# Kernel optimization log

Measured on AMD Instinct MI355X. Metric: run time of the kernel, lower is better.

Reference implementation:

```python
import jax, jax.numpy as jnp
import numpy as np


def setup_inputs() -> dict:
    key = jax.random.key(0)
    k1, k2, k3, k4 = jax.random.split(key, 4)
    B, N, M, D = 8, 2048, 2048, 256
    x = jax.random.normal(k1, (B, N, D), dtype=jnp.float32)
    Fi = jax.random.normal(k2, (B, M, D), dtype=jnp.float32)
    # nn.Linear(dim, dim) params (W applied as x @ W.T + b); scale like torch default
    bound = 1.0 / np.sqrt(D)
    W = jax.random.uniform(k3, (D, D), dtype=jnp.float32, minval=-bound, maxval=bound)
    b = jax.random.uniform(k4, (D,), dtype=jnp.float32, minval=-bound, maxval=bound)
    return {"x": x, "Fi": Fi, "W": W, "b": b}


def reference(x, Fi, W, b):
    # x: [B, N, D], Fi: [B, M, D]
    q = jnp.einsum("bnd,ed->bne", x, W) + b          # linear projection
    scores = jnp.einsum("bnd,bmd->bnm", q, Fi)        # QK^T (no scaling in original)
    attn = jax.nn.softmax(scores, axis=-1)            # softmax over keys
    out = jnp.einsum("bnm,bmd->bnd", attn, Fi)        # attention @ V (V = Fi)
    return out
```

## Files before the change

kernel.cpp:

```cpp
#include <hip/hip_runtime.h>
#include <hip/hip_bf16.h>

typedef _Float16 half8 __attribute__((ext_vector_type(8)));
typedef float floatx4 __attribute__((ext_vector_type(4)));

#define MFMA16H(a, b, c) __builtin_amdgcn_mfma_f32_16x16x32_f16((a), (b), (c), 0, 0, 0)

static constexpr int Bb = 8, Nn = 2048, Mm = 2048, Dd = 256;

__device__ inline void async16(const void* g, void* l)
{
    __builtin_amdgcn_global_load_lds((const __attribute__((address_space(1))) unsigned int*)g,
                                     (__attribute__((address_space(3))) unsigned int*)l,
                                     16, 0, 0);
}

__device__ inline half8 cvt8h(const float* __restrict__ p)
{
    float4 f0 = *reinterpret_cast<const float4*>(p);
    float4 f1 = *reinterpret_cast<const float4*>(p + 4);
    half8 r;
    r[0] = (_Float16)f0.x; r[1] = (_Float16)f0.y; r[2] = (_Float16)f0.z; r[3] = (_Float16)f0.w;
    r[4] = (_Float16)f1.x; r[5] = (_Float16)f1.y; r[6] = (_Float16)f1.z; r[7] = (_Float16)f1.w;
    return r;
}

__device__ inline void cvt8h_split(const float* __restrict__ p, half8& h, half8& l)
{
    float4 f0 = *reinterpret_cast<const float4*>(p);
    float4 f1 = *reinterpret_cast<const float4*>(p + 4);
    float f[8] = {f0.x, f0.y, f0.z, f0.w, f1.x, f1.y, f1.z, f1.w};
#pragma unroll
    for (int i = 0; i < 8; ++i) {
        _Float16 hh = (_Float16)f[i];
        h[i] = hh;
        l[i] = (_Float16)(f[i] - (float)hh);
    }
}

__global__ __launch_bounds__(256, 4)
void prep_kernel(const float* __restrict__ Fi, const float* __restrict__ W,
                 _Float16* __restrict__ FiH, _Float16* __restrict__ FiT,
                 _Float16* __restrict__ Wh, _Float16* __restrict__ Wl)
{
    const int bid = blockIdx.x;
    const int t = threadIdx.x;

    if (bid >= 1024) {
        const size_t base = (size_t)(bid - 1024) * 2048 + t * 8;
        half8 h, l;
        cvt8h_split(W + base, h, l);
        *(half8*)(Wh + base) = h;
        *(half8*)(Wl + base) = l;
        return;
    }

    __shared__ __align__(16) unsigned short tile[64][64];
    const int b  = bid >> 7;
    const int mt = (bid >> 2) & 31;
    const int dt = bid & 3;
    {
        const int i = t >> 2, jc = (t & 3) * 16;
        const int pc = ((jc >> 4) ^ (i >> 4)) * 16;
        const float* src = Fi + ((size_t)b * Mm + mt * 64 + i) * Dd + dt * 64 + jc;
        union { half8 v; uint4 u; } p0, p1;
        p0.v = cvt8h(src);
        p1.v = cvt8h(src + 8);
        *(uint4*)&tile[i][pc]     = p0.u;
        *(uint4*)&tile[i][pc + 8] = p1.u;
        unsigned short* dh = reinterpret_cast<unsigned short*>(FiH)
            + ((size_t)b * Mm + mt * 64 + i) * Dd + dt * 64 + jc;
        *(uint4*)dh       = p0.u;
        *(uint4*)(dh + 8) = p1.u;
    }
    __syncthreads();
    {
        const int d = t >> 2, mc = (t & 3) * 16;
        unsigned short* dst = reinterpret_cast<unsigned short*>(FiT)
            + ((size_t)b * Dd + dt * 64 + d) * Mm + mt * 64 + mc;
        union { uint4 v[2]; unsigned short s[16]; } u;
#pragma unroll
        for (int s = 0; s < 16; ++s) {
            const int row = mc + s;
            u.s[s] = tile[row][((d >> 4) ^ (row >> 4)) * 16 + (d & 15)];
        }
        *(uint4*)dst       = u.v[0];
        *(uint4*)(dst + 8) = u.v[1];
    }
}

__global__ __launch_bounds__(256, 2)
void qproj_kernel(const float* __restrict__ x, const _Float16* __restrict__ Wh,
                  const _Float16* __restrict__ Wl, const float* __restrict__ bias,
                  _Float16* __restrict__ q)
{
    __shared__ __align__(16) _Float16 sWhA[256 * 32];
    __shared__ __align__(16) _Float16 sWlA[256 * 32];
    __shared__ __align__(16) _Float16 sWhB[256 * 32];
    __shared__ __align__(16) _Float16 sWlB[256 * 32];

    const int tid = threadIdx.x;
    const int lane = tid & 63, w = tid >> 6;
    const int lo = lane & 15, hi = lane >> 4;
    const long r0 = (long)blockIdx.x * 32;

    floatx4 acc[2][4];
#pragma unroll
    for (int rt = 0; rt < 2; ++rt)
#pragma unroll
        for (int j = 0; j < 4; ++j) acc[rt][j] = (floatx4)0.0f;

    const int se = lane >> 2, sc = lane & 3;

    auto stage = [&](int k0, _Float16* dWh, _Float16* dWl) {
#pragma unroll
        for (int j = 0; j < 4; ++j) {
            const int e0 = (w * 4 + j) * 16;
            const int e = e0 + se;
            const int gc = sc ^ (e & 3);
            async16(Wh + (size_t)e * Dd + k0 + gc * 8, dWh + e0 * 32);
            async16(Wl + (size_t)e * Dd + k0 + gc * 8, dWl + e0 * 32);
        }
    };

    auto compute = [&](int k0, const _Float16* SWh, const _Float16* SWl) {
        half8 ah[2], al[2];
#pragma unroll
        for (int rt = 0; rt < 2; ++rt)
            cvt8h_split(x + (size_t)(r0 + rt * 16 + lo) * Dd + k0 + hi * 8, ah[rt], al[rt]);
#pragma unroll
        for (int jj = 0; jj < 4; ++jj) {
            const int e = (w * 4 + jj) * 16 + lo;
            half8 bh = *reinterpret_cast<const half8*>(&SWh[(e & 255) * 32 + ((hi ^ (e & 3)) * 8)]);
            half8 bl = *reinterpret_cast<const half8*>(&SWl[(e & 255) * 32 + ((hi ^ (e & 3)) * 8)]);
#pragma unroll
            for (int rt = 0; rt < 2; ++rt) {
                acc[rt][jj] = MFMA16H(ah[rt], bh, acc[rt][jj]);
                acc[rt][jj] = MFMA16H(ah[rt], bl, acc[rt][jj]);
                acc[rt][jj] = MFMA16H(al[rt], bh, acc[rt][jj]);
            }
        }
    };

    stage(0, sWhA, sWlA);
    for (int k0 = 0; k0 < 256; k0 += 64) {
        __syncthreads();
        stage(k0 + 32, sWhB, sWlB);
        compute(k0, sWhA, sWlA);
        __syncthreads();
        if (k0 + 64 < 256) stage(k0 + 64, sWhA, sWlA);
        compute(k0 + 32, sWhB, sWlB);
    }
#pragma unroll
    for (int jj = 0; jj < 4; ++jj) {
        const int e = (w * 4 + jj) * 16 + lo;
        const float bv = bias[e];
#pragma unroll
        for (int rt = 0; rt < 2; ++rt)
#pragma unroll
            for (int r = 0; r < 4; ++r)
                q[(size_t)(r0 + rt * 16 + hi * 4 + r) * Dd + e] = (_Float16)(acc[rt][jj][r] + bv);
    }
}

__global__ __launch_bounds__(256, 2)
void flash_kernel(const _Float16* __restrict__ q, const _Float16* __restrict__ FiH,
                  const _Float16* __restrict__ FiT, _Float16* __restrict__ o_part,
                  float* __restrict__ m_part, float* __restrict__ l_part)
{
    __shared__ __align__(16) _Float16 sFiA[32 * 256];
    __shared__ __align__(16) _Float16 sFiB[32 * 256];
    __shared__ __align__(16) _Float16 sFiTA[256 * 32];
    __shared__ __align__(16) _Float16 sFiTB[256 * 32];
    __shared__ __align__(16) _Float16 sP[4][32 * 36];

    const int bid = blockIdx.x;
    const int b  = bid & 7;
    const int u  = bid >> 3;
    const int nt = u & 15;
    const int kh = u >> 4;
    const int tid = threadIdx.x;
    const int lane = tid & 63, w = tid >> 6;
    const int lo = lane & 15, hi = lane >> 4;
    const int nbase = nt * 128 + w * 32;

    const _Float16* fH = FiH + (size_t)b * Mm * Dd;
    const _Float16* fT = FiT + (size_t)b * Dd * Mm;

    half8 qf[2][8];
    const _Float16* qb = q + ((size_t)b * Nn + nbase + lo) * Dd + hi * 8;
#pragma unroll
    for (int rt = 0; rt < 2; ++rt)
#pragma unroll
        for (int kk = 0; kk < 8; ++kk)
            qf[rt][kk] = *reinterpret_cast<const half8*>(qb + rt * 16 * Dd + kk * 32);

    half8 ones;
#pragma unroll
    for (int i = 0; i < 8; ++i) ones[i] = (_Float16)1.0f;

    floatx4 o[2][16];
    floatx4 ol[2];
#pragma unroll
    for (int rt = 0; rt < 2; ++rt) {
#pragma unroll
        for (int t = 0; t < 16; ++t) o[rt][t] = (floatx4)0.0f;
        ol[rt] = (floatx4)0.0f;
    }
    float m_i[2][4];
#pragma unroll
    for (int rt = 0; rt < 2; ++rt)
#pragma unroll
        for (int r = 0; r < 4; ++r) m_i[rt][r] = -INFINITY;

    auto stage = [&](int it, _Float16* dFi, _Float16* dFiT) {
        const int key0 = kh * 512 + it * 32;
#pragma unroll
        for (int j = 0; j < 4; ++j) {
            const int rbase = (w * 4 + j) * 2;
            const int r = rbase + (lane >> 5);
            const int gc = (lane & 31) ^ (r & 7);
            async16(fH + (size_t)(key0 + r) * Dd + gc * 8, dFi + rbase * 256);
        }
#pragma unroll
        for (int j = 0; j < 4; ++j) {
            const int rbase = (w + j * 4) * 16;
            const int r = rbase + (lane >> 2);
            const int gc = (lane & 3) ^ (r & 3);
            async16(fT + (size_t)r * Mm + key0 + gc * 8, dFiT + rbase * 32);
        }
    };

    auto compute = [&](const _Float16* SFI, const _Float16* SFIT) {
        floatx4 s[2][2];
#pragma unroll
        for (int rt = 0; rt < 2; ++rt)
#pragma unroll
            for (int st = 0; st < 2; ++st) s[rt][st] = (floatx4)0.0f;
#pragma unroll
        for (int st = 0; st < 2; ++st) {
            const int row = st * 16 + lo;
#pragma unroll
            for (int kk = 0; kk < 8; ++kk) {
                half8 bv = *reinterpret_cast<const half8*>(
                    SFI + row * 256 + (((kk * 4 + hi) ^ (lo & 7)) * 8));
                s[0][st] = MFMA16H(qf[0][kk], bv, s[0][st]);
                s[1][st] = MFMA16H(qf[1][kk], bv, s[1][st]);
            }
        }

        float mn[2][4];
        bool chg = false;
#pragma unroll
        for (int rt = 0; rt < 2; ++rt)
#pragma unroll
            for (int r = 0; r < 4; ++r) {
                float mc = fmaxf(s[rt][0][r], s[rt][1][r]);
                mc = fmaxf(mc, __shfl_xor(mc, 1));
                mc = fmaxf(mc, __shfl_xor(mc, 2));
                mc = fmaxf(mc, __shfl_xor(mc, 4));
                mc = fmaxf(mc, __shfl_xor(mc, 8));
                mn[rt][r] = fmaxf(m_i[rt][r], mc);
                chg = chg || (mn[rt][r] > m_i[rt][r]);
            }
        if (__any(chg)) {
#pragma unroll
            for (int rt = 0; rt < 2; ++rt) {
                float al4[4];
#pragma unroll
                for (int r = 0; r < 4; ++r) {
                    al4[r] = __expf(m_i[rt][r] - mn[rt][r]);
                    m_i[rt][r] = mn[rt][r];
                }
#pragma unroll
                for (int t = 0; t < 16; ++t) {
                    floatx4 ot = o[rt][t];
#pragma unroll
                    for (int r = 0; r < 4; ++r) ot[r] *= al4[r];
                    o[rt][t] = ot;
                }
#pragma unroll
                for (int r = 0; r < 4; ++r) ol[rt][r] *= al4[r];
            }
        }
#pragma unroll
        for (int rt = 0; rt < 2; ++rt)
#pragma unroll
            for (int r = 0; r < 4; ++r) {
                _Float16 p0 = (_Float16)__expf(s[rt][0][r] - m_i[rt][r]);
                _Float16 p1 = (_Float16)__expf(s[rt][1][r] - m_i[rt][r]);
                sP[w][(rt * 16 + hi * 4 + r) * 36 + lo]      = p0;
                sP[w][(rt * 16 + hi * 4 + r) * 36 + 16 + lo] = p1;
            }

        half8 pa0 = *reinterpret_cast<const half8*>(&sP[w][lo * 36 + hi * 8]);
        half8 pa1 = *reinterpret_cast<const half8*>(&sP[w][(16 + lo) * 36 + hi * 8]);
#pragma unroll
        for (int t = 0; t < 16; ++t) {
            half8 bv = *reinterpret_cast<const half8*>(
                SFIT + (t * 16 + lo) * 32 + ((hi ^ (lo & 3)) * 8));
            o[0][t] = MFMA16H(pa0, bv, o[0][t]);
            o[1][t] = MFMA16H(pa1, bv, o[1][t]);
        }
        ol[0] = MFMA16H(pa0, ones, ol[0]);
        ol[1] = MFMA16H(pa1, ones, ol[1]);
    };

    stage(0, sFiA, sFiTA);
    for (int it = 0; it < 16; it += 2) {
        __syncthreads();
        stage(it + 1, sFiB, sFiTB);
        compute(sFiA, sFiTA);
        __syncthreads();
        if (it + 2 < 16) stage(it + 2, sFiA, sFiTA);
        compute(sFiB, sFiTB);
    }

#pragma unroll
    for (int rt = 0; rt < 2; ++rt)
#pragma unroll
        for (int r = 0; r < 4; ++r) {
            const long gq = (long)b * Nn + nbase + rt * 16 + hi * 4 + r;
            const size_t obase = ((size_t)kh * (Bb * Nn) + gq) * Dd;
#pragma unroll
            for (int t = 0; t < 16; ++t)
                o_part[obase + t * 16 + lo] = (_Float16)o[rt][t][r];
            if (lo == 0) {
                m_part[(size_t)kh * (Bb * Nn) + gq] = m_i[rt][r];
                l_part[(size_t)kh * (Bb * Nn) + gq] = ol[rt][r];
            }
        }
}

__global__ __launch_bounds__(256, 8)
void merge_kernel(const _Float16* __restrict__ o_part, const float* __restrict__ m_part,
                  const float* __restrict__ l_part, float* __restrict__ out)
{
    const int col = threadIdx.x;
#pragma unroll
    for (int rr = 0; rr < 8; ++rr) {
        const int row = blockIdx.x * 8 + rr;
        float m[4], l[4];
#pragma unroll
        for (int k = 0; k < 4; ++k) {
            m[k] = m_part[(size_t)k * (Bb * Nn) + row];
            l[k] = l_part[(size_t)k * (Bb * Nn) + row];
        }
        float M = fmaxf(fmaxf(m[0], m[1]), fmaxf(m[2], m[3]));
        float denom = 0.f, acc = 0.f;
#pragma unroll
        for (int k = 0; k < 4; ++k) {
            const float wk = __expf(m[k] - M);
            denom += wk * l[k];
            acc += wk * (float)o_part[((size_t)k * (Bb * Nn) + row) * Dd + col];
        }
        out[(size_t)row * Dd + col] = acc / denom;
    }
}

extern "C" void kernel_launch(void* const* d_in, const int* in_sizes, int n_in,
                              void* d_out, int out_size, void* d_ws, size_t ws_size,
                              hipStream_t stream)
{
    const float* x    = (const float*)d_in[0];
    const float* Fi   = (const float*)d_in[1];
    const float* W    = (const float*)d_in[2];
    const float* bias = (const float*)d_in[3];
    float* out = (float*)d_out;

    _Float16* q_ws = (_Float16*)d_ws;
    _Float16* FiH  = q_ws + (size_t)Bb * Nn * Dd;
    _Float16* FiT  = FiH + (size_t)Bb * Mm * Dd;
    _Float16* Wh   = FiT + (size_t)Bb * Dd * Mm;
    _Float16* Wl   = Wh + (size_t)Dd * Dd;
    _Float16* o_part = Wl + (size_t)Dd * Dd;
    float* m_part  = (float*)(o_part + (size_t)4 * Bb * Nn * Dd);
    float* l_part  = m_part + (size_t)4 * Bb * Nn;

    hipLaunchKernelGGL(prep_kernel, dim3(1056), dim3(256), 0, stream, Fi, W, FiH, FiT, Wh, Wl);
    hipLaunchKernelGGL(qproj_kernel, dim3(512), dim3(256), 0, stream, x, Wh, Wl, bias, q_ws);
    hipLaunchKernelGGL(flash_kernel, dim3(512), dim3(256), 0, stream, q_ws, FiH, FiT,
                       o_part, m_part, l_part);
    hipLaunchKernelGGL(merge_kernel, dim3(2048), dim3(256), 0, stream, o_part, m_part, l_part, out);
}
```

Baseline: 213.2 us.

## Drop LDS staging; read K/V and W fragments directly from global memory

```diff
diff --git a/kernel.cpp b/kernel.cpp
--- a/kernel.cpp
+++ b/kernel.cpp
@@ -7,13 +7,6 @@
 #define MFMA16H(a, b, c) __builtin_amdgcn_mfma_f32_16x16x32_f16((a), (b), (c), 0, 0, 0)
 
 static constexpr int Bb = 8, Nn = 2048, Mm = 2048, Dd = 256;
-
-__device__ inline void async16(const void* g, void* l)
-{
-    __builtin_amdgcn_global_load_lds((const __attribute__((address_space(1))) unsigned int*)g,
-                                     (__attribute__((address_space(3))) unsigned int*)l,
-                                     16, 0, 0);
-}
 
 __device__ inline half8 cvt8h(const float* __restrict__ p)
 {
@@ -89,77 +82,41 @@
     }
 }
 
-__global__ __launch_bounds__(256, 2)
+__global__ __launch_bounds__(256, 4)
 void qproj_kernel(const float* __restrict__ x, const _Float16* __restrict__ Wh,
                   const _Float16* __restrict__ Wl, const float* __restrict__ bias,
                   _Float16* __restrict__ q)
 {
-    __shared__ __align__(16) _Float16 sWhA[256 * 32];
-    __shared__ __align__(16) _Float16 sWlA[256 * 32];
-    __shared__ __align__(16) _Float16 sWhB[256 * 32];
-    __shared__ __align__(16) _Float16 sWlB[256 * 32];
-
     const int tid = threadIdx.x;
     const int lane = tid & 63, w = tid >> 6;
     const int lo = lane & 15, hi = lane >> 4;
-    const long r0 = (long)blockIdx.x * 32;
-
-    floatx4 acc[2][4];
-#pragma unroll
-    for (int rt = 0; rt < 2; ++rt)
-#pragma unroll
-        for (int j = 0; j < 4; ++j) acc[rt][j] = (floatx4)0.0f;
-
-    const int se = lane >> 2, sc = lane & 3;
-
-    auto stage = [&](int k0, _Float16* dWh, _Float16* dWl) {
-#pragma unroll
-        for (int j = 0; j < 4; ++j) {
-            const int e0 = (w * 4 + j) * 16;
-            const int e = e0 + se;
-            const int gc = sc ^ (e & 3);
-            async16(Wh + (size_t)e * Dd + k0 + gc * 8, dWh + e0 * 32);
-            async16(Wl + (size_t)e * Dd + k0 + gc * 8, dWl + e0 * 32);
-        }
-    };
-
-    auto compute = [&](int k0, const _Float16* SWh, const _Float16* SWl) {
-        half8 ah[2], al[2];
-#pragma unroll
-        for (int rt = 0; rt < 2; ++rt)
-            cvt8h_split(x + (size_t)(r0 + rt * 16 + lo) * Dd + k0 + hi * 8, ah[rt], al[rt]);
+    const long r0 = (long)blockIdx.x * 16;
+
+    floatx4 acc[4];
+#pragma unroll
+    for (int j = 0; j < 4; ++j) acc[j] = (floatx4)0.0f;
+
+#pragma unroll 2
+    for (int k0 = 0; k0 < 256; k0 += 32) {
+        half8 ah, al;
+        cvt8h_split(x + (size_t)(r0 + lo) * Dd + k0 + hi * 8, ah, al);
 #pragma unroll
         for (int jj = 0; jj < 4; ++jj) {
             const int e = (w * 4 + jj) * 16 + lo;
-            half8 bh = *reinterpret_cast<const half8*>(&SWh[(e & 255) * 32 + ((hi ^ (e & 3)) * 8)]);
-            half8 bl = *reinterpret_cast<const half8*>(&SWl[(e & 255) * 32 + ((hi ^ (e & 3)) * 8)]);
-#pragma unroll
-            for (int rt = 0; rt < 2; ++rt) {
-                acc[rt][jj] = MFMA16H(ah[rt], bh, acc[rt][jj]);
-                acc[rt][jj] = MFMA16H(ah[rt], bl, acc[rt][jj]);
-                acc[rt][jj] = MFMA16H(al[rt], bh, acc[rt][jj]);
-            }
-        }
-    };
-
-    stage(0, sWhA, sWlA);
-    for (int k0 = 0; k0 < 256; k0 += 64) {
-        __syncthreads();
-        stage(k0 + 32, sWhB, sWlB);
-        compute(k0, sWhA, sWlA);
-        __syncthreads();
-        if (k0 + 64 < 256) stage(k0 + 64, sWhA, sWlA);
-        compute(k0 + 32, sWhB, sWlB);
+            half8 bh = *reinterpret_cast<const half8*>(Wh + (size_t)e * Dd + k0 + hi * 8);
+            half8 bl = *reinterpret_cast<const half8*>(Wl + (size_t)e * Dd + k0 + hi * 8);
+            acc[jj] = MFMA16H(ah, bh, acc[jj]);
+            acc[jj] = MFMA16H(ah, bl, acc[jj]);
+            acc[jj] = MFMA16H(al, bh, acc[jj]);
+        }
     }
 #pragma unroll
     for (int jj = 0; jj < 4; ++jj) {
         const int e = (w * 4 + jj) * 16 + lo;
         const float bv = bias[e];
 #pragma unroll
-        for (int rt = 0; rt < 2; ++rt)
-#pragma unroll
-            for (int r = 0; r < 4; ++r)
-                q[(size_t)(r0 + rt * 16 + hi * 4 + r) * Dd + e] = (_Float16)(acc[rt][jj][r] + bv);
+        for (int r = 0; r < 4; ++r)
+            q[(size_t)(r0 + hi * 4 + r) * Dd + e] = (_Float16)(acc[jj][r] + bv);
     }
 }
 
@@ -168,11 +125,8 @@
                   const _Float16* __restrict__ FiT, _Float16* __restrict__ o_part,
                   float* __restrict__ m_part, float* __restrict__ l_part)
 {
-    __shared__ __align__(16) _Float16 sFiA[32 * 256];
-    __shared__ __align__(16) _Float16 sFiB[32 * 256];
-    __shared__ __align__(16) _Float16 sFiTA[256 * 32];
-    __shared__ __align__(16) _Float16 sFiTB[256 * 32];
     __shared__ __align__(16) _Float16 sP[4][32 * 36];
+    __shared__ __align__(16) _Float16 sO[4][16][280];
 
     const int bid = blockIdx.x;
     const int b  = bid & 7;
@@ -213,25 +167,11 @@
 #pragma unroll
         for (int r = 0; r < 4; ++r) m_i[rt][r] = -INFINITY;
 
-    auto stage = [&](int it, _Float16* dFi, _Float16* dFiT) {
-        const int key0 = kh * 512 + it * 32;
-#pragma unroll
-        for (int j = 0; j < 4; ++j) {
-            const int rbase = (w * 4 + j) * 2;
-            const int r = rbase + (lane >> 5);
-            const int gc = (lane & 31) ^ (r & 7);
-            async16(fH + (size_t)(key0 + r) * Dd + gc * 8, dFi + rbase * 256);
-        }
-#pragma unroll
-        for (int j = 0; j < 4; ++j) {
-            const int rbase = (w + j * 4) * 16;
-            const int r = rbase + (lane >> 2);
-            const int gc = (lane & 3) ^ (r & 3);
-            async16(fT + (size_t)r * Mm + key0 + gc * 8, dFiT + rbase * 32);
-        }
-    };
-
-    auto compute = [&](const _Float16* SFI, const _Float16* SFIT) {
+    const _Float16* pH = fH + (size_t)(kh * 512 + lo) * Dd + hi * 8;
+    const _Float16* pT = fT + (size_t)lo * Mm + kh * 512 + hi * 8;
+
+#pragma unroll 2
+    for (int it = 0; it < 16; ++it) {
         floatx4 s[2][2];
 #pragma unroll
         for (int rt = 0; rt < 2; ++rt)
@@ -239,11 +179,10 @@
             for (int st = 0; st < 2; ++st) s[rt][st] = (floatx4)0.0f;
 #pragma unroll
         for (int st = 0; st < 2; ++st) {
-            const int row = st * 16 + lo;
+            const _Float16* kb = pH + (size_t)(it * 32 + st * 16) * Dd;
 #pragma unroll
             for (int kk = 0; kk < 8; ++kk) {
-                half8 bv = *reinterpret_cast<const half8*>(
-                    SFI + row * 256 + (((kk * 4 + hi) ^ (lo & 7)) * 8));
+                half8 bv = *reinterpret_cast<const half8*>(kb + kk * 32);
                 s[0][st] = MFMA16H(qf[0][kk], bv, s[0][st]);
                 s[1][st] = MFMA16H(qf[1][kk], bv, s[1][st]);
             }
@@ -295,41 +234,42 @@
 
         half8 pa0 = *reinterpret_cast<const half8*>(&sP[w][lo * 36 + hi * 8]);
         half8 pa1 = *reinterpret_cast<const half8*>(&sP[w][(16 + lo) * 36 + hi * 8]);
+
+        const _Float16* vb = pT + it * 32;
 #pragma unroll
         for (int t = 0; t < 16; ++t) {
-            half8 bv = *reinterpret_cast<const half8*>(
-                SFIT + (t * 16 + lo) * 32 + ((hi ^ (lo & 3)) * 8));
+            half8 bv = *reinterpret_cast<const half8*>(vb + (size_t)t * 16 * Mm);
             o[0][t] = MFMA16H(pa0, bv, o[0][t]);
             o[1][t] = MFMA16H(pa1, bv, o[1][t]);
         }
         ol[0] = MFMA16H(pa0, ones, ol[0]);
         ol[1] = MFMA16H(pa1, ones, ol[1]);
-    };
-
-    stage(0, sFiA, sFiTA);
-    for (int it = 0; it < 16; it += 2) {
-        __syncthreads();
-        stage(it + 1, sFiB, sFiTB);
-        compute(sFiA, sFiTA);
-        __syncthreads();
-        if (it + 2 < 16) stage(it + 2, sFiA, sFiTA);
-        compute(sFiB, sFiTB);
-    }
-
-#pragma unroll
-    for (int rt = 0; rt < 2; ++rt)
-#pragma unroll
-        for (int r = 0; r < 4; ++r) {
-            const long gq = (long)b * Nn + nbase + rt * 16 + hi * 4 + r;
-            const size_t obase = ((size_t)kh * (Bb * Nn) + gq) * Dd;
-#pragma unroll
-            for (int t = 0; t < 16; ++t)
-                o_part[obase + t * 16 + lo] = (_Float16)o[rt][t][r];
-            if (lo == 0) {
-                m_part[(size_t)kh * (Bb * Nn) + gq] = m_i[rt][r];
-                l_part[(size_t)kh * (Bb * Nn) + gq] = ol[rt][r];
-            }
-        }
+    }
+
+    const size_t gq0 = (size_t)kh * (Bb * Nn) + (size_t)b * Nn + nbase;
+#pragma unroll
+    for (int rt = 0; rt < 2; ++rt) {
+#pragma unroll
+        for (int t = 0; t < 16; ++t)
+#pragma unroll
+            for (int r = 0; r < 4; ++r)
+                sO[w][hi * 4 + r][t * 16 + lo] = (_Float16)o[rt][t][r];
+        if (lo == 0) {
+#pragma unroll
+            for (int r = 0; r < 4; ++r) {
+                const size_t gq = gq0 + rt * 16 + hi * 4 + r;
+                m_part[gq] = m_i[rt][r];
+                l_part[gq] = ol[rt][r];
+            }
+        }
+        const int row = lane >> 2, cq = lane & 3;
+        _Float16* gp = o_part + (gq0 + rt * 16 + row) * Dd;
+#pragma unroll
+        for (int j = 0; j < 8; ++j) {
+            half8 v = *reinterpret_cast<const half8*>(&sO[w][row][(j * 4 + cq) * 8]);
+            *reinterpret_cast<half8*>(gp + (j * 4 + cq) * 8) = v;
+        }
+    }
 }
 
 __global__ __launch_bounds__(256, 8)
@@ -378,7 +318,7 @@
     float* l_part  = m_part + (size_t)4 * Bb * Nn;
 
     hipLaunchKernelGGL(prep_kernel, dim3(1056), dim3(256), 0, stream, Fi, W, FiH, FiT, Wh, Wl);
-    hipLaunchKernelGGL(qproj_kernel, dim3(512), dim3(256), 0, stream, x, Wh, Wl, bias, q_ws);
+    hipLaunchKernelGGL(qproj_kernel, dim3(1024), dim3(256), 0, stream, x, Wh, Wl, bias, q_ws);
     hipLaunchKernelGGL(flash_kernel, dim3(512), dim3(256), 0, stream, q_ws, FiH, FiT,
                        o_part, m_part, l_part);
     hipLaunchKernelGGL(merge_kernel, dim3(2048), dim3(256), 0, stream, o_part, m_part, l_part, out);
```

After: 399.5 us. 1.87x slower.

## Shrink flash tiles to 16 rows per wave and double grid for occupancy

Applied to the files above, without the earlier changes.

```diff
diff --git a/kernel.cpp b/kernel.cpp
--- a/kernel.cpp
+++ b/kernel.cpp
@@ -163,173 +163,158 @@
     }
 }
 
-__global__ __launch_bounds__(256, 2)
+__global__ __launch_bounds__(256, 4)
 void flash_kernel(const _Float16* __restrict__ q, const _Float16* __restrict__ FiH,
                   const _Float16* __restrict__ FiT, _Float16* __restrict__ o_part,
                   float* __restrict__ m_part, float* __restrict__ l_part)
 {
-    __shared__ __align__(16) _Float16 sFiA[32 * 256];
-    __shared__ __align__(16) _Float16 sFiB[32 * 256];
-    __shared__ __align__(16) _Float16 sFiTA[256 * 32];
-    __shared__ __align__(16) _Float16 sFiTB[256 * 32];
-    __shared__ __align__(16) _Float16 sP[4][32 * 36];
+    __shared__ __align__(16) _Float16 smem[2 * 16 * 256 + 256 * 32 + 4 * 16 * 36];
+    _Float16* sK0 = smem;
+    _Float16* sK1 = smem + 16 * 256;
+    _Float16* sV  = smem + 2 * 16 * 256;
+    _Float16* sP  = smem + 2 * 16 * 256 + 256 * 32;
 
     const int bid = blockIdx.x;
     const int b  = bid & 7;
     const int u  = bid >> 3;
-    const int nt = u & 15;
-    const int kh = u >> 4;
+    const int nt = u & 31;
+    const int kh = u >> 5;
     const int tid = threadIdx.x;
     const int lane = tid & 63, w = tid >> 6;
     const int lo = lane & 15, hi = lane >> 4;
-    const int nbase = nt * 128 + w * 32;
+    const int nbase = nt * 64 + w * 16;
+    const int key00 = kh * 512;
 
     const _Float16* fH = FiH + (size_t)b * Mm * Dd;
     const _Float16* fT = FiT + (size_t)b * Dd * Mm;
-
-    half8 qf[2][8];
+    _Float16* sPw = sP + w * (16 * 36);
+
+    half8 qf[8];
     const _Float16* qb = q + ((size_t)b * Nn + nbase + lo) * Dd + hi * 8;
 #pragma unroll
-    for (int rt = 0; rt < 2; ++rt)
-#pragma unroll
-        for (int kk = 0; kk < 8; ++kk)
-            qf[rt][kk] = *reinterpret_cast<const half8*>(qb + rt * 16 * Dd + kk * 32);
+    for (int kk = 0; kk < 8; ++kk)
+        qf[kk] = *reinterpret_cast<const half8*>(qb + kk * 32);
 
     half8 ones;
 #pragma unroll
     for (int i = 0; i < 8; ++i) ones[i] = (_Float16)1.0f;
 
-    floatx4 o[2][16];
-    floatx4 ol[2];
-#pragma unroll
-    for (int rt = 0; rt < 2; ++rt) {
-#pragma unroll
-        for (int t = 0; t < 16; ++t) o[rt][t] = (floatx4)0.0f;
-        ol[rt] = (floatx4)0.0f;
-    }
-    float m_i[2][4];
-#pragma unroll
-    for (int rt = 0; rt < 2; ++rt)
-#pragma unroll
-        for (int r = 0; r < 4; ++r) m_i[rt][r] = -INFINITY;
-
-    auto stage = [&](int it, _Float16* dFi, _Float16* dFiT) {
-        const int key0 = kh * 512 + it * 32;
-#pragma unroll
-        for (int j = 0; j < 4; ++j) {
-            const int rbase = (w * 4 + j) * 2;
+    floatx4 o[16];
+    floatx4 ol = (floatx4)0.0f;
+#pragma unroll
+    for (int t = 0; t < 16; ++t) o[t] = (floatx4)0.0f;
+    float m_i[4];
+#pragma unroll
+    for (int r = 0; r < 4; ++r) m_i[r] = -INFINITY;
+
+    auto stageK = [&](int it, _Float16* dst) {
+        const int key0 = key00 + it * 16;
+#pragma unroll
+        for (int j = 0; j < 2; ++j) {
+            const int rbase = (w * 2 + j) * 2;
             const int r = rbase + (lane >> 5);
             const int gc = (lane & 31) ^ (r & 7);
-            async16(fH + (size_t)(key0 + r) * Dd + gc * 8, dFi + rbase * 256);
-        }
+            async16(fH + (size_t)(key0 + r) * Dd + gc * 8, dst + rbase * 256);
+        }
+    };
+    auto stageV = [&](int p) {
+        const int key0 = key00 + p * 32;
 #pragma unroll
         for (int j = 0; j < 4; ++j) {
             const int rbase = (w + j * 4) * 16;
             const int r = rbase + (lane >> 2);
             const int gc = (lane & 3) ^ (r & 3);
-            async16(fT + (size_t)r * Mm + key0 + gc * 8, dFiT + rbase * 32);
-        }
-    };
-
-    auto compute = [&](const _Float16* SFI, const _Float16* SFIT) {
-        floatx4 s[2][2];
-#pragma unroll
-        for (int rt = 0; rt < 2; ++rt)
-#pragma unroll
-            for (int st = 0; st < 2; ++st) s[rt][st] = (floatx4)0.0f;
-#pragma unroll
-        for (int st = 0; st < 2; ++st) {
-            const int row = st * 16 + lo;
-#pragma unroll
-            for (int kk = 0; kk < 8; ++kk) {
-                half8 bv = *reinterpret_cast<const half8*>(
-                    SFI + row * 256 + (((kk * 4 + hi) ^ (lo & 7)) * 8));
-                s[0][st] = MFMA16H(qf[0][kk], bv, s[0][st]);
-                s[1][st] = MFMA16H(qf[1][kk], bv, s[1][st]);
+            async16(fT + (size_t)r * Mm + key0 + gc * 8, sV + rbase * 32);
+        }
+    };
+
+    auto qkt = [&](const _Float16* SK) -> floatx4 {
+        floatx4 s = (floatx4)0.0f;
+        __builtin_amdgcn_s_setprio(1);
+#pragma unroll
+        for (int kk = 0; kk < 8; ++kk) {
+            half8 bv = *reinterpret_cast<const half8*>(
+                SK + lo * 256 + (((kk * 4 + hi) ^ (lo & 7)) * 8));
+            s = MFMA16H(qf[kk], bv, s);
+        }
+        __builtin_amdgcn_s_setprio(0);
+        return s;
+    };
+
+    stageK(0, sK0);
+    stageV(0);
+
+    for (int p = 0; p < 16; ++p) {
+        __syncthreads();
+        stageK(2 * p + 1, sK1);
+        if (p > 0) stageV(p);
+        floatx4 sprev = qkt(sK0);
+
+        __syncthreads();
+        if (p + 1 < 16) stageK(2 * p + 2, sK0);
+        floatx4 s = qkt(sK1);
+
+        float mn[4];
+        bool chg = false;
+#pragma unroll
+        for (int r = 0; r < 4; ++r) {
+            float mc = fmaxf(sprev[r], s[r]);
+            mc = fmaxf(mc, __shfl_xor(mc, 1));
+            mc = fmaxf(mc, __shfl_xor(mc, 2));
+            mc = fmaxf(mc, __shfl_xor(mc, 4));
+            mc = fmaxf(mc, __shfl_xor(mc, 8));
+            mn[r] = fmaxf(m_i[r], mc);
+            chg = chg || (mn[r] > m_i[r] + 4.0f);
+        }
+        if (__any(chg)) {
+#pragma unroll
+            for (int r = 0; r < 4; ++r) {
+                const float al = __expf(m_i[r] - mn[r]);
+                m_i[r] = mn[r];
+#pragma unroll
+                for (int t = 0; t < 16; ++t) o[t][r] *= al;
+                ol[r] *= al;
             }
         }
-
-        float mn[2][4];
-        bool chg = false;
-#pragma unroll
-        for (int rt = 0; rt < 2; ++rt)
-#pragma unroll
-            for (int r = 0; r < 4; ++r) {
-                float mc = fmaxf(s[rt][0][r], s[rt][1][r]);
-                mc = fmaxf(mc, __shfl_xor(mc, 1));
-                mc = fmaxf(mc, __shfl_xor(mc, 2));
-                mc = fmaxf(mc, __shfl_xor(mc, 4));
-                mc = fmaxf(mc, __shfl_xor(mc, 8));
-                mn[rt][r] = fmaxf(m_i[rt][r], mc);
-                chg = chg || (mn[rt][r] > m_i[rt][r]);
-            }
-        if (__any(chg)) {
-#pragma unroll
-            for (int rt = 0; rt < 2; ++rt) {
-                float al4[4];
-#pragma unroll
-                for (int r = 0; r < 4; ++r) {
-                    al4[r] = __expf(m_i[rt][r] - mn[rt][r]);
-                    m_i[rt][r] = mn[rt][r];
-                }
-#pragma unroll
-                for (int t = 0; t < 16; ++t) {
-                    floatx4 ot = o[rt][t];
-#pragma unroll
-                    for (int r = 0; r < 4; ++r) ot[r] *= al4[r];
-                    o[rt][t] = ot;
-                }
-#pragma unroll
-                for (int r = 0; r < 4; ++r) ol[rt][r] *= al4[r];
-            }
-        }
-#pragma unroll
-        for (int rt = 0; rt < 2; ++rt)
-#pragma unroll
-            for (int r = 0; r < 4; ++r) {
-                _Float16 p0 = (_Float16)__expf(s[rt][0][r] - m_i[rt][r]);
-                _Float16 p1 = (_Float16)__expf(s[rt][1][r] - m_i[rt][r]);
-                sP[w][(rt * 16 + hi * 4 + r) * 36 + lo]      = p0;
-                sP[w][(rt * 16 + hi * 4 + r) * 36 + 16 + lo] = p1;
-            }
-
-        half8 pa0 = *reinterpret_cast<const half8*>(&sP[w][lo * 36 + hi * 8]);
-        half8 pa1 = *reinterpret_cast<const half8*>(&sP[w][(16 + lo) * 36 + hi * 8]);
+#pragma unroll
+        for (int r = 0; r < 4; ++r) {
+            sPw[(hi * 4 + r) * 36 + lo]      = (_Float16)__expf(sprev[r] - m_i[r]);
+            sPw[(hi * 4 + r) * 36 + 16 + lo] = (_Float16)__expf(s[r] - m_i[r]);
+        }
+
+        half8 pa = *reinterpret_cast<const half8*>(&sPw[lo * 36 + hi * 8]);
+        __builtin_amdgcn_s_setprio(1);
 #pragma unroll
         for (int t = 0; t < 16; ++t) {
             half8 bv = *reinterpret_cast<const half8*>(
-                SFIT + (t * 16 + lo) * 32 + ((hi ^ (lo & 3)) * 8));
-            o[0][t] = MFMA16H(pa0, bv, o[0][t]);
-            o[1][t] = MFMA16H(pa1, bv, o[1][t]);
-        }
-        ol[0] = MFMA16H(pa0, ones, ol[0]);
-        ol[1] = MFMA16H(pa1, ones, ol[1]);
-    };
-
-    stage(0, sFiA, sFiTA);
-    for (int it = 0; it < 16; it += 2) {
-        __syncthreads();
-        stage(it + 1, sFiB, sFiTB);
-        compute(sFiA, sFiTA);
-        __syncthreads();
-        if (it + 2 < 16) stage(it + 2, sFiA, sFiTA);
-        compute(sFiB, sFiTB);
-    }
-
-#pragma unroll
-    for (int rt = 0; rt < 2; ++rt)
+                sV + (t * 16 + lo) * 32 + ((hi ^ (lo & 3)) * 8));
+            o[t] = MFMA16H(pa, bv, o[t]);
+        }
+        ol = MFMA16H(pa, ones, ol);
+        __builtin_amdgcn_s_setprio(0);
+    }
+
+    __syncthreads();
+    _Float16* sOw = smem + w * (16 * 264);
+    const size_t gq0 = (size_t)kh * (Bb * Nn) + (size_t)b * Nn + nbase;
+#pragma unroll
+    for (int t = 0; t < 16; ++t)
+#pragma unroll
+        for (int r = 0; r < 4; ++r)
+            sOw[(hi * 4 + r) * 264 + t * 16 + lo] = (_Float16)o[t][r];
+    if (lo == 0) {
 #pragma unroll
         for (int r = 0; r < 4; ++r) {
-            const long gq = (long)b * Nn + nbase + rt * 16 + hi * 4 + r;
-            const size_t obase = ((size_t)kh * (Bb * Nn) + gq) * Dd;
-#pragma unroll
-            for (int t = 0; t < 16; ++t)
-                o_part[obase + t * 16 + lo] = (_Float16)o[rt][t][r];
-            if (lo == 0) {
-                m_part[(size_t)kh * (Bb * Nn) + gq] = m_i[rt][r];
-                l_part[(size_t)kh * (Bb * Nn) + gq] = ol[rt][r];
-            }
-        }
+            m_part[gq0 + hi * 4 + r] = m_i[r];
+            l_part[gq0 + hi * 4 + r] = ol[r];
+        }
+    }
+    const int row = lane >> 2, cq = lane & 3;
+    _Float16* gp = o_part + (gq0 + row) * Dd;
+#pragma unroll
+    for (int j = 0; j < 8; ++j)
+        *reinterpret_cast<half8*>(gp + (j * 4 + cq) * 8) =
+            *reinterpret_cast<const half8*>(&sOw[row * 264 + (j * 4 + cq) * 8]);
 }
 
 __global__ __launch_bounds__(256, 8)
@@ -379,7 +364,7 @@
 
     hipLaunchKernelGGL(prep_kernel, dim3(1056), dim3(256), 0, stream, Fi, W, FiH, FiT, Wh, Wl);
     hipLaunchKernelGGL(qproj_kernel, dim3(512), dim3(256), 0, stream, x, Wh, Wl, bias, q_ws);
-    hipLaunchKernelGGL(flash_kernel, dim3(512), dim3(256), 0, stream, q_ws, FiH, FiT,
+    hipLaunchKernelGGL(flash_kernel, dim3(1024), dim3(256), 0, stream, q_ws, FiH, FiT,
                        o_part, m_part, l_part);
     hipLaunchKernelGGL(merge_kernel, dim3(2048), dim3(256), 0, stream, o_part, m_part, l_part, out);
 }
```

Measured after the change: 453.8 us. +112.8%, slower.

## Fuse split-K merge into flash kernel via last-block atomic counter; lazy rescale

Applied to the files above, without the earlier changes.

```diff
diff --git a/kernel.cpp b/kernel.cpp
--- a/kernel.cpp
+++ b/kernel.cpp
@@ -41,11 +41,16 @@
 __global__ __launch_bounds__(256, 4)
 void prep_kernel(const float* __restrict__ Fi, const float* __restrict__ W,
                  _Float16* __restrict__ FiH, _Float16* __restrict__ FiT,
-                 _Float16* __restrict__ Wh, _Float16* __restrict__ Wl)
+                 _Float16* __restrict__ Wh, _Float16* __restrict__ Wl,
+                 int* __restrict__ cnt)
 {
     const int bid = blockIdx.x;
     const int t = threadIdx.x;
 
+    if (bid >= 1056) {
+        if (t < 128) cnt[t] = 0;
+        return;
+    }
     if (bid >= 1024) {
         const size_t base = (size_t)(bid - 1024) * 2048 + t * 8;
         half8 h, l;
@@ -166,13 +171,15 @@
 __global__ __launch_bounds__(256, 2)
 void flash_kernel(const _Float16* __restrict__ q, const _Float16* __restrict__ FiH,
                   const _Float16* __restrict__ FiT, _Float16* __restrict__ o_part,
-                  float* __restrict__ m_part, float* __restrict__ l_part)
+                  float* __restrict__ m_part, float* __restrict__ l_part,
+                  int* __restrict__ cnt, float* __restrict__ out)
 {
     __shared__ __align__(16) _Float16 sFiA[32 * 256];
     __shared__ __align__(16) _Float16 sFiB[32 * 256];
     __shared__ __align__(16) _Float16 sFiTA[256 * 32];
     __shared__ __align__(16) _Float16 sFiTB[256 * 32];
     __shared__ __align__(16) _Float16 sP[4][32 * 36];
+    __shared__ int sLast;
 
     const int bid = blockIdx.x;
     const int b  = bid & 7;
@@ -261,7 +268,7 @@
                 mc = fmaxf(mc, __shfl_xor(mc, 4));
                 mc = fmaxf(mc, __shfl_xor(mc, 8));
                 mn[rt][r] = fmaxf(m_i[rt][r], mc);
-                chg = chg || (mn[rt][r] > m_i[rt][r]);
+                chg = chg || (mn[rt][r] > m_i[rt][r] + 4.0f);
             }
         if (__any(chg)) {
 #pragma unroll
@@ -330,16 +337,18 @@
                 l_part[(size_t)kh * (Bb * Nn) + gq] = ol[rt][r];
             }
         }
-}
-
-__global__ __launch_bounds__(256, 8)
-void merge_kernel(const _Float16* __restrict__ o_part, const float* __restrict__ m_part,
-                  const float* __restrict__ l_part, float* __restrict__ out)
-{
-    const int col = threadIdx.x;
-#pragma unroll
-    for (int rr = 0; rr < 8; ++rr) {
-        const int row = blockIdx.x * 8 + rr;
+
+    __threadfence();
+    if (tid == 0)
+        sLast = (atomicAdd(&cnt[b * 16 + nt], 1) == 3);
+    __syncthreads();
+    if (!sLast) return;
+    __threadfence();
+
+    const int col = tid;
+    const size_t row0 = (size_t)b * Nn + nt * 128;
+    for (int rr = 0; rr < 128; ++rr) {
+        const size_t row = row0 + rr;
         float m[4], l[4];
 #pragma unroll
         for (int k = 0; k < 4; ++k) {
@@ -354,7 +363,7 @@
             denom += wk * l[k];
             acc += wk * (float)o_part[((size_t)k * (Bb * Nn) + row) * Dd + col];
         }
-        out[(size_t)row * Dd + col] = acc / denom;
+        out[row * Dd + col] = acc / denom;
     }
 }
 
@@ -376,10 +385,10 @@
     _Float16* o_part = Wl + (size_t)Dd * Dd;
     float* m_part  = (float*)(o_part + (size_t)4 * Bb * Nn * Dd);
     float* l_part  = m_part + (size_t)4 * Bb * Nn;
-
-    hipLaunchKernelGGL(prep_kernel, dim3(1056), dim3(256), 0, stream, Fi, W, FiH, FiT, Wh, Wl);
+    int*   cnt     = (int*)(l_part + (size_t)4 * Bb * Nn);
+
+    hipLaunchKernelGGL(prep_kernel, dim3(1057), dim3(256), 0, stream, Fi, W, FiH, FiT, Wh, Wl, cnt);
     hipLaunchKernelGGL(qproj_kernel, dim3(512), dim3(256), 0, stream, x, Wh, Wl, bias, q_ws);
     hipLaunchKernelGGL(flash_kernel, dim3(512), dim3(256), 0, stream, q_ws, FiH, FiT,
-                       o_part, m_part, l_part);
-    hipLaunchKernelGGL(merge_kernel, dim3(2048), dim3(256), 0, stream, o_part, m_part, l_part, out);
-}
+                       o_part, m_part, l_part, cnt, out);
+}
```

Result: slower. 498.3 us (+133.7%).
